# Performance work log

Hardware: AMD Instinct MI355X
Metric: run time of the kernel (lower is better)

## Reference

```python
import jax, jax.numpy as jnp
import numpy as np

N_NODES = 50000
N_EDGES = 800000
D = 128
NEG_SLOPE = 0.2  # PyG GATConv default negative_slope
PRESERVE = 0.1


def _gat_conv(x, src, dst, W, a_src, a_dst, bias, n_nodes):
    """PyG GATConv with heads=1, concat=False, edge_dim=None (eval mode, no dropout)."""
    h = x @ W                              # [N, D] transformed features
    alpha_s = h @ a_src                    # [N] per-node source score
    alpha_d = h @ a_dst                    # [N] per-node dest score
    e = jax.nn.leaky_relu(alpha_s[src] + alpha_d[dst], NEG_SLOPE)  # [E]
    # segment softmax over incoming edges of each dst node
    m = jax.ops.segment_max(e, dst, num_segments=n_nodes)          # [N]
    ex = jnp.exp(e - m[dst])                                       # [E]
    s = jax.ops.segment_sum(ex, dst, num_segments=n_nodes)         # [N]
    alpha = ex / (s[dst] + 1e-16)                                  # [E]
    out = jax.ops.segment_sum(alpha[:, None] * h[src], dst, num_segments=n_nodes)
    return out + bias


def setup_inputs() -> dict:
    key = jax.random.key(0)
    ks = jax.random.split(key, 12)
    sc = 1.0 / np.sqrt(D)
    return {
        "skill_embed": jax.random.normal(ks[0], (N_NODES, D), dtype=jnp.float32),
        "adj_list": jax.random.randint(ks[1], (2, N_EDGES), 0, N_NODES, dtype=jnp.int64),
        "edge_attr": jax.random.normal(ks[2], (N_EDGES,), dtype=jnp.float32),
        "W1": jax.random.normal(ks[3], (D, D), dtype=jnp.float32) * sc,
        "a_src1": jax.random.normal(ks[4], (D,), dtype=jnp.float32) * sc,
        "a_dst1": jax.random.normal(ks[5], (D,), dtype=jnp.float32) * sc,
        "b1": jnp.zeros((D,), dtype=jnp.float32),
        "W2": jax.random.normal(ks[6], (D, D), dtype=jnp.float32) * sc,
        "a_src2": jax.random.normal(ks[7], (D,), dtype=jnp.float32) * sc,
        "a_dst2": jax.random.normal(ks[8], (D,), dtype=jnp.float32) * sc,
        "b2": jnp.zeros((D,), dtype=jnp.float32),
    }


def reference(skill_embed, adj_list, edge_attr, W1, a_src1, a_dst1, b1, W2, a_src2, a_dst2, b2):
    n = skill_embed.shape[0]
    src, dst = adj_list[0], adj_list[1]
    # edge_attr is ignored by GATConv when edge_dim=None (as in the source module)
    t = _gat_conv(skill_embed, src, dst, W1, a_src1, a_dst1, b1, n)
    t = jax.nn.relu(PRESERVE * skill_embed + (1.0 - PRESERVE) * t)
    out = _gat_conv(t, src, dst, W2, a_src2, a_dst2, b2, n)
    return out
```

## Files before the change

### kernel.cpp

```cpp
#include <hip/hip_runtime.h>
#include <hip/hip_bf16.h>

#define N_NODES 50000
#define N_EDGES 800000
#define D 128


__global__ void count_kernel(const int* __restrict__ adj, int* __restrict__ deg) {
    int e = blockIdx.x * blockDim.x + threadIdx.x;
    if (e < N_EDGES) {
        int d = adj[N_EDGES + e];
        atomicAdd(&deg[d], 1);
    }
}


__global__ void scan1_kernel(const int* __restrict__ deg, int* __restrict__ rowptr,
                             int* __restrict__ parts) {
    __shared__ int sm[256];
    int i = blockIdx.x * 256 + threadIdx.x;
    int v = (i < N_NODES) ? deg[i] : 0;
    sm[threadIdx.x] = v;
    __syncthreads();
    for (int off = 1; off < 256; off <<= 1) {
        int t = (threadIdx.x >= off) ? sm[threadIdx.x - off] : 0;
        __syncthreads();
        sm[threadIdx.x] += t;
        __syncthreads();
    }
    if (i < N_NODES) rowptr[i] = sm[threadIdx.x] - v;
    if (threadIdx.x == 255) parts[blockIdx.x] = sm[255];
}

__global__ void scan2_kernel(int* parts, int nb) {
    __shared__ int sm[256];
    int v = (threadIdx.x < nb) ? parts[threadIdx.x] : 0;
    sm[threadIdx.x] = v;
    __syncthreads();
    for (int off = 1; off < 256; off <<= 1) {
        int t = (threadIdx.x >= off) ? sm[threadIdx.x - off] : 0;
        __syncthreads();
        sm[threadIdx.x] += t;
        __syncthreads();
    }
    if (threadIdx.x < nb) parts[threadIdx.x] = sm[threadIdx.x] - v;
}

__global__ void scan3_kernel(int* __restrict__ rowptr, const int* __restrict__ parts,
                             int* __restrict__ cursor) {
    int i = blockIdx.x * 256 + threadIdx.x;
    if (i < N_NODES) {
        int v = rowptr[i] + parts[i >> 8];
        rowptr[i] = v;
        cursor[i] = v;
    }
    if (i == 0) rowptr[N_NODES] = N_EDGES;
}

__global__ void scatter_kernel(const int* __restrict__ adj, int* __restrict__ cursor,
                               int* __restrict__ ssrc, int* __restrict__ sdst) {
    int e = blockIdx.x * blockDim.x + threadIdx.x;
    if (e < N_EDGES) {
        int d = adj[N_EDGES + e];
        int p = atomicAdd(&cursor[d], 1);
        ssrc[p] = adj[e];
        sdst[p] = d;
    }
}


__global__ __launch_bounds__(256) void edgew_kernel(
        const int* __restrict__ ssrc, const int* __restrict__ sdst,
        const float* __restrict__ AS, const float* __restrict__ AD,
        float* __restrict__ ew) {
    int e = blockIdx.x * 256 + threadIdx.x;
    if (e < N_EDGES) {
        float v = AS[ssrc[e]] + AD[sdst[e]];
        v = (v > 0.f) ? v : 0.2f * v;
        ew[e] = __expf(v);
    }
}


#define BK 32
#define XT_S 68
#define WT_S 132

__global__ __launch_bounds__(256, 4) void gemm_kernel(
        const float* __restrict__ X, const float* __restrict__ W,
        const float* __restrict__ a_src, const float* __restrict__ a_dst,
        float* __restrict__ H, float* __restrict__ AS, float* __restrict__ AD) {
    __shared__ float xt[BK * XT_S];
    __shared__ float wt[BK * WT_S];
    int tid = threadIdx.x;
    int rg = tid >> 5;
    int cg = tid & 31;
    int row0 = blockIdx.x * 64;

    float4 acc[8];
#pragma unroll
    for (int j = 0; j < 8; ++j) acc[j] = make_float4(0.f, 0.f, 0.f, 0.f);

    for (int ks = 0; ks < 4; ++ks) {
        int k0 = ks * BK;
        {
            const float4* Wv = (const float4*)(W + (size_t)k0 * D);
            float4* wt4 = (float4*)wt;
#pragma unroll
            for (int i = 0; i < 4; ++i) {
                int f = tid + 256 * i;
                int k = f >> 5, c4 = f & 31;
                wt4[k * 33 + c4] = Wv[k * 32 + c4];
            }
        }
#pragma unroll
        for (int i = 0; i < 2; ++i) {
            int f = tid + 256 * i;
            int r = f >> 3, fi = f & 7;
            int gr = row0 + r; gr = (gr < N_NODES) ? gr : (N_NODES - 1);
            float4 xv = *(const float4*)&X[(size_t)gr * D + k0 + fi * 4];
            xt[(fi * 4 + 0) * XT_S + r] = xv.x;
            xt[(fi * 4 + 1) * XT_S + r] = xv.y;
            xt[(fi * 4 + 2) * XT_S + r] = xv.z;
            xt[(fi * 4 + 3) * XT_S + r] = xv.w;
        }
        __syncthreads();
#pragma unroll
        for (int k = 0; k < BK; ++k) {
            float4 xa = *(const float4*)&xt[k * XT_S + rg * 8];
            float4 xb = *(const float4*)&xt[k * XT_S + rg * 8 + 4];
            float4 wv = *(const float4*)&wt[k * WT_S + cg * 4];
            float xr[8] = {xa.x, xa.y, xa.z, xa.w, xb.x, xb.y, xb.z, xb.w};
#pragma unroll
            for (int j = 0; j < 8; ++j) {
                acc[j].x = fmaf(xr[j], wv.x, acc[j].x);
                acc[j].y = fmaf(xr[j], wv.y, acc[j].y);
                acc[j].z = fmaf(xr[j], wv.z, acc[j].z);
                acc[j].w = fmaf(xr[j], wv.w, acc[j].w);
            }
        }
        __syncthreads();
    }

    float4 asv = *(const float4*)&a_src[cg * 4];
    float4 adv = *(const float4*)&a_dst[cg * 4];
#pragma unroll
    for (int j = 0; j < 8; ++j) {
        int r = row0 + rg * 8 + j;
        if (r < N_NODES) *(float4*)&H[(size_t)r * D + cg * 4] = acc[j];
        float pa = acc[j].x * asv.x + acc[j].y * asv.y + acc[j].z * asv.z + acc[j].w * asv.w;
        float pd = acc[j].x * adv.x + acc[j].y * adv.y + acc[j].z * adv.z + acc[j].w * adv.w;
#pragma unroll
        for (int off = 16; off > 0; off >>= 1) {
            pa += __shfl_xor(pa, off);
            pd += __shfl_xor(pd, off);
        }
        if (cg == 0 && r < N_NODES) { AS[r] = pa; AD[r] = pd; }
    }
}


template <int LAYER>
__global__ __launch_bounds__(256, 8) void agg_kernel(
        const float* __restrict__ H, const float* __restrict__ ew,
        const int* __restrict__ rowptr, const int* __restrict__ ssrc,
        const float* __restrict__ bias, const float* __restrict__ Xskip,
        float* __restrict__ OUT) {
    int pair = threadIdx.x >> 7;
    int sub  = (threadIdx.x >> 6) & 1;
    int l    = threadIdx.x & 63;
    int node = blockIdx.x * 2 + pair;

    __shared__ float cacc[2][128];
    __shared__ float cs[2];

    int e0 = rowptr[node], e1 = rowptr[node + 1];
    int emid = (e0 + e1) >> 1;
    int lo = sub ? emid : e0;
    int hi = sub ? e1 : emid;

    float2 acc = make_float2(0.f, 0.f);
    float s = 0.f;

    while (lo + 8 <= hi) {
        int sn[8]; float wg[8]; float2 hv[8];
#pragma unroll
        for (int i = 0; i < 8; ++i) { sn[i] = ssrc[lo + i]; wg[i] = ew[lo + i]; }
#pragma unroll
        for (int i = 0; i < 8; ++i) hv[i] = *(const float2*)&H[(size_t)sn[i] * D + 2 * l];
#pragma unroll
        for (int i = 0; i < 8; ++i) {
            s += wg[i];
            acc.x = fmaf(wg[i], hv[i].x, acc.x);
            acc.y = fmaf(wg[i], hv[i].y, acc.y);
        }
        lo += 8;
    }
    if (lo + 4 <= hi) {
        int sn[4]; float wg[4]; float2 hv[4];
#pragma unroll
        for (int i = 0; i < 4; ++i) { sn[i] = ssrc[lo + i]; wg[i] = ew[lo + i]; }
#pragma unroll
        for (int i = 0; i < 4; ++i) hv[i] = *(const float2*)&H[(size_t)sn[i] * D + 2 * l];
#pragma unroll
        for (int i = 0; i < 4; ++i) {
            s += wg[i];
            acc.x = fmaf(wg[i], hv[i].x, acc.x);
            acc.y = fmaf(wg[i], hv[i].y, acc.y);
        }
        lo += 4;
    }
    for (; lo < hi; ++lo) {
        int sn = ssrc[lo]; float wg = ew[lo];
        float2 hv = *(const float2*)&H[(size_t)sn * D + 2 * l];
        s += wg;
        acc.x = fmaf(wg, hv.x, acc.x);
        acc.y = fmaf(wg, hv.y, acc.y);
    }

    if (sub == 1) {
        cacc[pair][2 * l]     = acc.x;
        cacc[pair][2 * l + 1] = acc.y;
        if (l == 0) cs[pair] = s;
    }
    __syncthreads();
    if (sub == 0) {
        acc.x += cacc[pair][2 * l];
        acc.y += cacc[pair][2 * l + 1];
        s += cs[pair];
        float inv = 1.f / (s + 1e-16f);
        float2 bv = ((const float2*)bias)[l];
        float o0 = acc.x * inv + bv.x;
        float o1 = acc.y * inv + bv.y;
        if (LAYER == 1) {
            float2 xs = *(const float2*)&Xskip[(size_t)node * D + 2 * l];
            o0 = fmaxf(0.1f * xs.x + 0.9f * o0, 0.f);
            o1 = fmaxf(0.1f * xs.y + 0.9f * o1, 0.f);
        }
        *(float2*)&OUT[(size_t)node * D + 2 * l] = make_float2(o0, o1);
    }
}


extern "C" void kernel_launch(void* const* d_in, const int* in_sizes, int n_in,
                              void* d_out, int out_size, void* d_ws, size_t ws_size,
                              hipStream_t stream) {
    const float* x   = (const float*)d_in[0];
    const int*   adj = (const int*)d_in[1];
    const float* W1  = (const float*)d_in[3];
    const float* as1 = (const float*)d_in[4];
    const float* ad1 = (const float*)d_in[5];
    const float* b1  = (const float*)d_in[6];
    const float* W2  = (const float*)d_in[7];
    const float* as2 = (const float*)d_in[8];
    const float* ad2 = (const float*)d_in[9];
    const float* b2  = (const float*)d_in[10];
    float* out = (float*)d_out;

    char* ws = (char*)d_ws;
    size_t off = 0;
    auto alloc = [&](size_t bytes) -> void* {
        void* p = ws + off;
        off = (off + bytes + 255) & ~(size_t)255;
        return p;
    };
    float* H      = (float*)alloc((size_t)N_NODES * D * 4);
    float* AS     = (float*)alloc((size_t)N_NODES * 4);
    float* AD     = (float*)alloc((size_t)N_NODES * 4);
    int*   deg    = (int*)alloc((size_t)N_NODES * 4);
    int*   rowptr = (int*)alloc((size_t)(N_NODES + 1) * 4);
    int*   cursor = (int*)alloc((size_t)N_NODES * 4);
    int*   ssrc   = (int*)alloc((size_t)N_EDGES * 4);
    int*   sdst   = (int*)alloc((size_t)N_EDGES * 4);
    float* ew     = (float*)alloc((size_t)N_EDGES * 4);
    int*   parts  = (int*)alloc(256 * 4);
    float* T      = out;

    const int EB = (N_EDGES + 255) / 256;
    const int NB = (N_NODES + 255) / 256;

    hipMemsetAsync(deg, 0, (size_t)N_NODES * 4, stream);
    count_kernel<<<EB, 256, 0, stream>>>(adj, deg);
    scan1_kernel<<<NB, 256, 0, stream>>>(deg, rowptr, parts);
    scan2_kernel<<<1, 256, 0, stream>>>(parts, NB);
    scan3_kernel<<<NB, 256, 0, stream>>>(rowptr, parts, cursor);
    scatter_kernel<<<EB, 256, 0, stream>>>(adj, cursor, ssrc, sdst);

    const int GB = (N_NODES + 63) / 64;
    const int AB = N_NODES / 2;

    gemm_kernel<<<GB, 256, 0, stream>>>(x, W1, as1, ad1, H, AS, AD);
    edgew_kernel<<<EB, 256, 0, stream>>>(ssrc, sdst, AS, AD, ew);
    agg_kernel<1><<<AB, 256, 0, stream>>>(H, ew, rowptr, ssrc, b1, x, T);
    gemm_kernel<<<GB, 256, 0, stream>>>(T, W2, as2, ad2, H, AS, AD);
    edgew_kernel<<<EB, 256, 0, stream>>>(ssrc, sdst, AS, AD, ew);
    agg_kernel<2><<<AB, 256, 0, stream>>>(H, ew, rowptr, ssrc, b2, nullptr, out);
}
```

Before: 379.4 us.

## Fuse edge-weight computation into aggregation, one wave per node, prefetch GEMM tiles

Removes the separate edge-weight kernel and the sdst/ew buffers. Aggregation now computes leaky-relu and exp of AS[src]+AD[dst] inline, and assigns one 64-lane wave per destination node with a 16-wide unrolled gather and a masked tail, replacing the two-half split that merged through shared memory. The GEMM gains register double-buffering so the next k-slice loads from global memory while the current one is computed. The cost is redundant exp work across the 64 lanes, more registers per thread (launch bounds lowered to 4), and less parallelism per node for high-degree nodes.

```diff
diff --git a/kernel.cpp b/kernel.cpp
--- a/kernel.cpp
+++ b/kernel.cpp
@@ -58,26 +58,12 @@
 }
 
 __global__ void scatter_kernel(const int* __restrict__ adj, int* __restrict__ cursor,
-                               int* __restrict__ ssrc, int* __restrict__ sdst) {
+                               int* __restrict__ ssrc) {
     int e = blockIdx.x * blockDim.x + threadIdx.x;
     if (e < N_EDGES) {
         int d = adj[N_EDGES + e];
         int p = atomicAdd(&cursor[d], 1);
         ssrc[p] = adj[e];
-        sdst[p] = d;
-    }
-}
-
-
-__global__ __launch_bounds__(256) void edgew_kernel(
-        const int* __restrict__ ssrc, const int* __restrict__ sdst,
-        const float* __restrict__ AS, const float* __restrict__ AD,
-        float* __restrict__ ew) {
-    int e = blockIdx.x * 256 + threadIdx.x;
-    if (e < N_EDGES) {
-        float v = AS[ssrc[e]] + AD[sdst[e]];
-        v = (v > 0.f) ? v : 0.2f * v;
-        ew[e] = __expf(v);
     }
 }
 
@@ -101,30 +87,46 @@
 #pragma unroll
     for (int j = 0; j < 8; ++j) acc[j] = make_float4(0.f, 0.f, 0.f, 0.f);
 
-    for (int ks = 0; ks < 4; ++ks) {
-        int k0 = ks * BK;
-        {
-            const float4* Wv = (const float4*)(W + (size_t)k0 * D);
-            float4* wt4 = (float4*)wt;
-#pragma unroll
-            for (int i = 0; i < 4; ++i) {
-                int f = tid + 256 * i;
-                int k = f >> 5, c4 = f & 31;
-                wt4[k * 33 + c4] = Wv[k * 32 + c4];
-            }
-        }
+    float4 wreg[4], xreg[2];
+    auto loadw = [&](int ks) {
+        const float4* Wv = (const float4*)(W + (size_t)ks * BK * D);
+#pragma unroll
+        for (int i = 0; i < 4; ++i) {
+            int f = tid + 256 * i;
+            wreg[i] = Wv[(f >> 5) * 32 + (f & 31)];
+        }
+    };
+    auto loadx = [&](int ks) {
 #pragma unroll
         for (int i = 0; i < 2; ++i) {
             int f = tid + 256 * i;
             int r = f >> 3, fi = f & 7;
             int gr = row0 + r; gr = (gr < N_NODES) ? gr : (N_NODES - 1);
-            float4 xv = *(const float4*)&X[(size_t)gr * D + k0 + fi * 4];
-            xt[(fi * 4 + 0) * XT_S + r] = xv.x;
-            xt[(fi * 4 + 1) * XT_S + r] = xv.y;
-            xt[(fi * 4 + 2) * XT_S + r] = xv.z;
-            xt[(fi * 4 + 3) * XT_S + r] = xv.w;
-        }
-        __syncthreads();
+            xreg[i] = *(const float4*)&X[(size_t)gr * D + ks * BK + fi * 4];
+        }
+    };
+
+    loadw(0); loadx(0);
+    for (int ks = 0; ks < 4; ++ks) {
+        {
+            float4* wt4 = (float4*)wt;
+#pragma unroll
+            for (int i = 0; i < 4; ++i) {
+                int f = tid + 256 * i;
+                wt4[(f >> 5) * 33 + (f & 31)] = wreg[i];
+            }
+#pragma unroll
+            for (int i = 0; i < 2; ++i) {
+                int f = tid + 256 * i;
+                int r = f >> 3, fi = f & 7;
+                xt[(fi * 4 + 0) * XT_S + r] = xreg[i].x;
+                xt[(fi * 4 + 1) * XT_S + r] = xreg[i].y;
+                xt[(fi * 4 + 2) * XT_S + r] = xreg[i].z;
+                xt[(fi * 4 + 3) * XT_S + r] = xreg[i].w;
+            }
+        }
+        __syncthreads();
+        if (ks < 3) { loadw(ks + 1); loadx(ks + 1); }
 #pragma unroll
         for (int k = 0; k < BK; ++k) {
             float4 xa = *(const float4*)&xt[k * XT_S + rg * 8];
@@ -161,84 +163,74 @@
 
 
 template <int LAYER>
-__global__ __launch_bounds__(256, 8) void agg_kernel(
-        const float* __restrict__ H, const float* __restrict__ ew,
+__global__ __launch_bounds__(256, 4) void agg_kernel(
+        const float* __restrict__ H, const float* __restrict__ AS,
+        const float* __restrict__ AD,
         const int* __restrict__ rowptr, const int* __restrict__ ssrc,
         const float* __restrict__ bias, const float* __restrict__ Xskip,
         float* __restrict__ OUT) {
-    int pair = threadIdx.x >> 7;
-    int sub  = (threadIdx.x >> 6) & 1;
+    int wave = threadIdx.x >> 6;
     int l    = threadIdx.x & 63;
-    int node = blockIdx.x * 2 + pair;
-
-    __shared__ float cacc[2][128];
-    __shared__ float cs[2];
+    int node = blockIdx.x * 4 + wave;
 
     int e0 = rowptr[node], e1 = rowptr[node + 1];
-    int emid = (e0 + e1) >> 1;
-    int lo = sub ? emid : e0;
-    int hi = sub ? e1 : emid;
-
+    float adn = AD[node];
     float2 acc = make_float2(0.f, 0.f);
     float s = 0.f;
-
-    while (lo + 8 <= hi) {
-        int sn[8]; float wg[8]; float2 hv[8];
-#pragma unroll
-        for (int i = 0; i < 8; ++i) { sn[i] = ssrc[lo + i]; wg[i] = ew[lo + i]; }
-#pragma unroll
-        for (int i = 0; i < 8; ++i) hv[i] = *(const float2*)&H[(size_t)sn[i] * D + 2 * l];
-#pragma unroll
-        for (int i = 0; i < 8; ++i) {
-            s += wg[i];
-            acc.x = fmaf(wg[i], hv[i].x, acc.x);
-            acc.y = fmaf(wg[i], hv[i].y, acc.y);
-        }
-        lo += 8;
-    }
-    if (lo + 4 <= hi) {
-        int sn[4]; float wg[4]; float2 hv[4];
-#pragma unroll
-        for (int i = 0; i < 4; ++i) { sn[i] = ssrc[lo + i]; wg[i] = ew[lo + i]; }
-#pragma unroll
-        for (int i = 0; i < 4; ++i) hv[i] = *(const float2*)&H[(size_t)sn[i] * D + 2 * l];
-#pragma unroll
-        for (int i = 0; i < 4; ++i) {
-            s += wg[i];
-            acc.x = fmaf(wg[i], hv[i].x, acc.x);
-            acc.y = fmaf(wg[i], hv[i].y, acc.y);
-        }
-        lo += 4;
-    }
-    for (; lo < hi; ++lo) {
-        int sn = ssrc[lo]; float wg = ew[lo];
-        float2 hv = *(const float2*)&H[(size_t)sn * D + 2 * l];
-        s += wg;
-        acc.x = fmaf(wg, hv.x, acc.x);
-        acc.y = fmaf(wg, hv.y, acc.y);
-    }
-
-    if (sub == 1) {
-        cacc[pair][2 * l]     = acc.x;
-        cacc[pair][2 * l + 1] = acc.y;
-        if (l == 0) cs[pair] = s;
-    }
-    __syncthreads();
-    if (sub == 0) {
-        acc.x += cacc[pair][2 * l];
-        acc.y += cacc[pair][2 * l + 1];
-        s += cs[pair];
-        float inv = 1.f / (s + 1e-16f);
-        float2 bv = ((const float2*)bias)[l];
-        float o0 = acc.x * inv + bv.x;
-        float o1 = acc.y * inv + bv.y;
-        if (LAYER == 1) {
-            float2 xs = *(const float2*)&Xskip[(size_t)node * D + 2 * l];
-            o0 = fmaxf(0.1f * xs.x + 0.9f * o0, 0.f);
-            o1 = fmaxf(0.1f * xs.y + 0.9f * o1, 0.f);
-        }
-        *(float2*)&OUT[(size_t)node * D + 2 * l] = make_float2(o0, o1);
-    }
+    int lo = e0;
+
+    while (lo + 16 <= e1) {
+        int sn[16]; float asv[16]; float2 hv[16];
+#pragma unroll
+        for (int i = 0; i < 16; ++i) sn[i] = ssrc[lo + i];
+#pragma unroll
+        for (int i = 0; i < 16; ++i) asv[i] = AS[sn[i]];
+#pragma unroll
+        for (int i = 0; i < 16; ++i) hv[i] = *(const float2*)&H[(size_t)sn[i] * D + 2 * l];
+#pragma unroll
+        for (int i = 0; i < 16; ++i) {
+            float v = asv[i] + adn;
+            v = (v > 0.f) ? v : 0.2f * v;
+            float w = __expf(v);
+            s += w;
+            acc.x = fmaf(w, hv[i].x, acc.x);
+            acc.y = fmaf(w, hv[i].y, acc.y);
+        }
+        lo += 16;
+    }
+    if (lo < e1) {
+        int n = e1 - lo;
+        int sn[16]; float asv[16]; float2 hv[16];
+#pragma unroll
+        for (int i = 0; i < 16; ++i) {
+            int e = lo + ((i < n) ? i : (n - 1));
+            sn[i] = ssrc[e];
+        }
+#pragma unroll
+        for (int i = 0; i < 16; ++i) asv[i] = AS[sn[i]];
+#pragma unroll
+        for (int i = 0; i < 16; ++i) hv[i] = *(const float2*)&H[(size_t)sn[i] * D + 2 * l];
+#pragma unroll
+        for (int i = 0; i < 16; ++i) {
+            float v = asv[i] + adn;
+            v = (v > 0.f) ? v : 0.2f * v;
+            float w = (i < n) ? __expf(v) : 0.f;
+            s += w;
+            acc.x = fmaf(w, hv[i].x, acc.x);
+            acc.y = fmaf(w, hv[i].y, acc.y);
+        }
+    }
+
+    float inv = 1.f / (s + 1e-16f);
+    float2 bv = ((const float2*)bias)[l];
+    float o0 = acc.x * inv + bv.x;
+    float o1 = acc.y * inv + bv.y;
+    if (LAYER == 1) {
+        float2 xs = *(const float2*)&Xskip[(size_t)node * D + 2 * l];
+        o0 = fmaxf(0.1f * xs.x + 0.9f * o0, 0.f);
+        o1 = fmaxf(0.1f * xs.y + 0.9f * o1, 0.f);
+    }
+    *(float2*)&OUT[(size_t)node * D + 2 * l] = make_float2(o0, o1);
 }
 
 
@@ -271,8 +263,6 @@
     int*   rowptr = (int*)alloc((size_t)(N_NODES + 1) * 4);
     int*   cursor = (int*)alloc((size_t)N_NODES * 4);
     int*   ssrc   = (int*)alloc((size_t)N_EDGES * 4);
-    int*   sdst   = (int*)alloc((size_t)N_EDGES * 4);
-    float* ew     = (float*)alloc((size_t)N_EDGES * 4);
     int*   parts  = (int*)alloc(256 * 4);
     float* T      = out;
 
@@ -284,15 +274,13 @@
     scan1_kernel<<<NB, 256, 0, stream>>>(deg, rowptr, parts);
     scan2_kernel<<<1, 256, 0, stream>>>(parts, NB);
     scan3_kernel<<<NB, 256, 0, stream>>>(rowptr, parts, cursor);
-    scatter_kernel<<<EB, 256, 0, stream>>>(adj, cursor, ssrc, sdst);
+    scatter_kernel<<<EB, 256, 0, stream>>>(adj, cursor, ssrc);
 
     const int GB = (N_NODES + 63) / 64;
-    const int AB = N_NODES / 2;
+    const int AB = (N_NODES + 3) / 4;
 
     gemm_kernel<<<GB, 256, 0, stream>>>(x, W1, as1, ad1, H, AS, AD);
-    edgew_kernel<<<EB, 256, 0, stream>>>(ssrc, sdst, AS, AD, ew);
-    agg_kernel<1><<<AB, 256, 0, stream>>>(H, ew, rowptr, ssrc, b1, x, T);
+    agg_kernel<1><<<AB, 256, 0, stream>>>(H, AS, AD, rowptr, ssrc, b1, x, T);
     gemm_kernel<<<GB, 256, 0, stream>>>(T, W2, as2, ad2, H, AS, AD);
-    edgew_kernel<<<EB, 256, 0, stream>>>(ssrc, sdst, AS, AD, ew);
-    agg_kernel<2><<<AB, 256, 0, stream>>>(H, ew, rowptr, ssrc, b2, nullptr, out);
-}
+    agg_kernel<2><<<AB, 256, 0, stream>>>(H, AS, AD, rowptr, ssrc, b2, nullptr, out);
+}
```

Measured after the change: 377.3 us. No clear change (-0.6%).
